# Kernel tuning notes

Measured on AMD Instinct MI355X. Metric: run time of the kernel, lower is better.

The kernel has to match this reference:

```python
import jax, jax.numpy as jnp
import numpy as np

B, NG, GS, D, L, NDL = 16, 50, 20, 256, 3, 2
N = NG * GS  # 1000


def setup_inputs() -> dict:
    key = jax.random.key(0)
    ks = jax.random.split(key, 8)
    amino_embd = jax.random.normal(ks[0], (B, NG, GS, D), dtype=jnp.float32)
    c = (jax.random.uniform(ks[1], (B, N, N)) < 0.02).astype(jnp.float32)
    prot_contacts = jnp.clip(c + jnp.transpose(c, (0, 2, 1)), 0.0, 1.0)
    # small init for bilinear W (original: random_uniform ~ +/-0.05) keeps exp() stable
    W_list = 0.01 * jax.random.normal(ks[2], (L, D, D), dtype=jnp.float32)
    dense_W = jax.random.normal(ks[3], (L, NDL, D, D), dtype=jnp.float32) / np.sqrt(D)
    dense_b = jnp.zeros((L, NDL, D), dtype=jnp.float32)
    final_W = jax.random.normal(ks[4], (D, D), dtype=jnp.float32) / np.sqrt(D)
    final_b = jnp.zeros((D,), dtype=jnp.float32)
    return {"amino_embd": amino_embd, "prot_contacts": prot_contacts,
            "W_list": W_list, "dense_W": dense_W, "dense_b": dense_b,
            "final_W": final_W, "final_b": final_b}


def reference(amino_embd, prot_contacts, W_list, dense_W, dense_b, final_W, final_b):
    dt = amino_embd.dtype
    eye = jnp.eye(N, dtype=dt)
    A = prot_contacts + eye  # contact map with self loops, [B,N,N]
    x = amino_embd.reshape(B, N, D)
    for l in range(L):
        x0 = x
        # bilinear non-local scores: [B,N,N]
        scores = jnp.einsum('bid,de,bje->bij', x0, W_list[l], x0)
        s = jnp.exp(scores) + jnp.asarray(1e-5, dt) * eye
        s = s * A                                   # mask by contacts + self loop
        s = s / jnp.sum(s, axis=-1, keepdims=True)  # row-normalize
        x = jnp.einsum('bij,bjd->bid', s, x0)       # aggregate
        for dl in range(NDL):
            x = jax.nn.relu(x @ dense_W[l, dl] + dense_b[l, dl])
        x = x + x0  # skip connection
    x = x @ final_W + final_b
    return x.reshape(B, NG, GS, D)
```

## Files before the change

### kernel.cpp

```cpp
#include <hip/hip_runtime.h>

#define BB 16
#define NN 1000
#define DD 256
#define LL 3
#define MAXNZ 256
#define MROWS (BB * NN)
#define SPLIT_SCALE 2048.0f
#define INV_SPLIT 4.8828125e-4f

typedef _Float16 f16x8 __attribute__((ext_vector_type(8)));
typedef _Float16 f16x2 __attribute__((ext_vector_type(2)));
typedef float f32x4 __attribute__((ext_vector_type(4)));

union H8 { f16x8 v; f16x2 p[4]; _Float16 h[8]; int4 i4; };

#if defined(__has_builtin)
#if __has_builtin(__builtin_amdgcn_fdot2)
#define HAS_FDOT2 1
#endif
#endif

__device__ __forceinline__ float dot2f(f16x2 a, f16x2 b, float c) {
#ifdef HAS_FDOT2
    return __builtin_amdgcn_fdot2(a, b, c, false);
#else
    return fmaf((float)a[0], (float)b[0], fmaf((float)a[1], (float)b[1], c));
#endif
}

__global__ __launch_bounds__(256) void convert_w(
    const float* __restrict__ W_list, const float* __restrict__ dense_W,
    const float* __restrict__ final_W,
    _Float16* __restrict__ wt_hi, _Float16* __restrict__ wt_lo)
{
    __shared__ float T[64][68];
    int blk = blockIdx.x;
    int mat = blk >> 4;
    int tile = blk & 15;
    int tk = (tile >> 2) * 64, tn = (tile & 3) * 64;
    const float* src = (mat < 3) ? (W_list + (size_t)mat * 65536)
                     : (mat < 9) ? (dense_W + (size_t)(mat - 3) * 65536)
                                 : final_W;
    int t = threadIdx.x;
    {
        int k = t >> 2, nc = (t & 3) * 16;
        const float* sp = src + (size_t)(tk + k) * 256 + tn + nc;
        *(float4*)&T[k][nc + 0]  = *(const float4*)(sp + 0);
        *(float4*)&T[k][nc + 4]  = *(const float4*)(sp + 4);
        *(float4*)&T[k][nc + 8]  = *(const float4*)(sp + 8);
        *(float4*)&T[k][nc + 12] = *(const float4*)(sp + 12);
    }
    __syncthreads();
    int n = t >> 2, kc = (t & 3) * 16;
    H8 hh0, hh1, ll0, ll1;
    #pragma unroll
    for (int i = 0; i < 16; ++i) {
        float x = T[kc + i][n];
        _Float16 hi = (_Float16)x;
        _Float16 lo = (_Float16)((x - (float)hi) * SPLIT_SCALE);
        if (i < 8) { hh0.h[i] = hi; ll0.h[i] = lo; }
        else       { hh1.h[i - 8] = hi; ll1.h[i - 8] = lo; }
    }
    size_t o = (size_t)mat * 65536 + (size_t)(tn + n) * 256 + tk + kc;
    *(int4*)(wt_hi + o)     = hh0.i4;
    *(int4*)(wt_hi + o + 8) = hh1.i4;
    *(int4*)(wt_lo + o)     = ll0.i4;
    *(int4*)(wt_lo + o + 8) = ll1.i4;
}

__global__ __launch_bounds__(256) void convert_x(
    const float* __restrict__ in, _Float16* __restrict__ hi,
    _Float16* __restrict__ lo)
{
    size_t gid = (size_t)blockIdx.x * 256 + threadIdx.x;
    const float* p = in + gid * 8;
    float4 a = *(const float4*)p;
    float4 b = *(const float4*)(p + 4);
    float xs[8] = {a.x, a.y, a.z, a.w, b.x, b.y, b.z, b.w};
    H8 hh, ll;
    #pragma unroll
    for (int i = 0; i < 8; ++i) {
        _Float16 h = (_Float16)xs[i];
        hh.h[i] = h;
        ll.h[i] = (_Float16)((xs[i] - (float)h) * SPLIT_SCALE);
    }
    *(int4*)(hi + gid * 8) = hh.i4;
    *(int4*)(lo + gid * 8) = ll.i4;
}

__global__ __launch_bounds__(256) void build_sparse(
    const float* __restrict__ contacts,
    int* __restrict__ idx, int* __restrict__ cnt, float* __restrict__ adiag)
{
    int wave = (int)((blockIdx.x * blockDim.x + threadIdx.x) >> 6);
    int lane = threadIdx.x & 63;
    if (wave >= MROWS) return;
    int b = wave / NN;
    int i = wave - b * NN;
    const float* row = contacts + (size_t)b * NN * NN + (size_t)i * NN;
    int* out = idx + (size_t)wave * MAXNZ;
    int count = 0;
    for (int j0 = 0; j0 < NN; j0 += 64) {
        int j = j0 + lane;
        float v = (j < NN) ? row[j] : 0.0f;
        bool p = (v != 0.0f) && (j != i);
        unsigned long long bal = __ballot(p);
        if (p) {
            int pre = __popcll(bal & ((1ull << lane) - 1ull));
            out[count + pre] = j;
        }
        count += __popcll(bal);
    }
    if (lane == 0) {
        cnt[wave] = count;
        adiag[wave] = row[i] + 1.0f;
    }
}

__global__ __launch_bounds__(256) void sparse_agg(
    const _Float16* __restrict__ yhi,
    const _Float16* __restrict__ xhi, const _Float16* __restrict__ xlo,
    const int* __restrict__ idx, const int* __restrict__ cnt,
    const float* __restrict__ adiag,
    _Float16* __restrict__ ohi, _Float16* __restrict__ olo)
{
    int bid = blockIdx.x;
    int xcd = bid & 7;
    int chunk = bid >> 3;
    int row = xcd * 2000 + chunk * 4 + (int)(threadIdx.x >> 6);
    row = __builtin_amdgcn_readfirstlane(row);
    int lane = threadIdx.x & 63;
    int g = lane >> 4, s = lane & 15;
    int b = row / NN;

    const _Float16* yp = yhi + (size_t)row * DD + s * 8;
    H8 yh0, yh1;
    yh0.i4 = *(const int4*)yp;
    yh1.i4 = *(const int4*)(yp + 128);

    const _Float16* xph = xhi + (size_t)row * DD + s * 8;
    const _Float16* xpl = xlo + (size_t)row * DD + s * 8;
    H8 xih0, xih1, xil0, xil1;
    xih0.i4 = *(const int4*)xph;       xih1.i4 = *(const int4*)(xph + 128);
    xil0.i4 = *(const int4*)xpl;       xil1.i4 = *(const int4*)(xpl + 128);
    float xi[16];
    #pragma unroll
    for (int u = 0; u < 8; ++u) {
        xi[u]     = fmaf((float)xil0.h[u], INV_SPLIT, (float)xih0.h[u]);
        xi[8 + u] = fmaf((float)xil1.h[u], INV_SPLIT, (float)xih1.h[u]);
    }
    const _Float16* xb = xhi + (size_t)b * NN * DD;

    float p = 0.0f;
    #pragma unroll
    for (int u = 0; u < 8; ++u) {
        p = fmaf((float)yh0.h[u], xi[u], p);
        p = fmaf((float)yh1.h[u], xi[8 + u], p);
    }
    p += __shfl_xor(p, 1); p += __shfl_xor(p, 2);
    p += __shfl_xor(p, 4); p += __shfl_xor(p, 8);
    float wd = (g == 0) ? (__expf(p) + 1e-5f) * adiag[row] : 0.0f;
    float denom = wd;
    float acc[16];
    #pragma unroll
    for (int u = 0; u < 16; ++u) acc[u] = wd * xi[u];

    const int c = cnt[row];
    const int* ip = idx + (size_t)row * MAXNZ;
    const int iters = (c + 3) >> 2;

    int j0 = (g < c) ? ip[g] : 0;
    int j1 = (4 + g < c) ? ip[4 + g] : 0;
    bool vok = g < c;
    H8 v0, v1;
    {
        const _Float16* xp = xb + (size_t)j0 * DD + s * 8;
        v0.i4 = *(const int4*)xp;
        v1.i4 = *(const int4*)(xp + 128);
    }

    for (int t = 0; t < iters; ++t) {
        int k2 = (t + 2) * 4 + g;
        int j2 = (k2 < c) ? ip[k2] : 0;
        H8 n0, n1;
        const _Float16* np = xb + (size_t)j1 * DD + s * 8;
        n0.i4 = *(const int4*)np;
        n1.i4 = *(const int4*)(np + 128);

        float q = 0.0f;
        #pragma unroll
        for (int i = 0; i < 4; ++i) q = dot2f(yh0.p[i], v0.p[i], q);
        #pragma unroll
        for (int i = 0; i < 4; ++i) q = dot2f(yh1.p[i], v1.p[i], q);
        q += __shfl_xor(q, 1); q += __shfl_xor(q, 2);
        q += __shfl_xor(q, 4); q += __shfl_xor(q, 8);
        float w = vok ? __expf(q) : 0.0f;
        denom += w;
        #pragma unroll
        for (int u = 0; u < 8; ++u) {
            acc[u]     = fmaf(w, (float)v0.h[u], acc[u]);
            acc[8 + u] = fmaf(w, (float)v1.h[u], acc[8 + u]);
        }

        v0 = n0; v1 = n1;
        j1 = j2;
        vok = (t + 1) * 4 + g < c;
    }

#define XG(x) x += __shfl_xor(x, 16); x += __shfl_xor(x, 32);
    XG(denom);
    #pragma unroll
    for (int u = 0; u < 16; ++u) { XG(acc[u]) }
#undef XG

    float inv = 1.0f / denom;
    int half = (g & 1) * 8;
    H8 st;
    #pragma unroll
    for (int i = 0; i < 8; ++i) {
        float x = acc[half + i] * inv;
        _Float16 h = (_Float16)x;
        st.h[i] = (g & 2) ? (_Float16)((x - (float)h) * SPLIT_SCALE) : h;
    }
    _Float16* dst = ((g & 2) ? olo : ohi) + (size_t)row * DD + (g & 1) * 128 + s * 8;
    *(int4*)dst = st.i4;
}

__global__ __launch_bounds__(256, 3) void gemm16(
    const _Float16* __restrict__ Ahi, const _Float16* __restrict__ Alo,
    const _Float16* __restrict__ Bhi, const _Float16* __restrict__ Blo,
    const float* __restrict__ bias,
    const _Float16* __restrict__ Shi, const _Float16* __restrict__ Slo,
    _Float16* __restrict__ Chi, _Float16* __restrict__ Clo,
    float* __restrict__ Cf32, int relu)
{
    __shared__ __align__(16) char smem[49152];
    char* Ah = smem;
    char* Al = smem + 8192;
    char* Bh = smem + 16384;
    char* Bl = smem + 32768;

    int tid = threadIdx.x;
    int mBase = blockIdx.y * 64;
    int nBase = blockIdx.x * 128;

    int sm = tid >> 2, kc = (tid & 3) * 16;
    int sb = tid >> 1, kcb = (tid & 1) * 32;
    const _Float16* gAh = Ahi + (size_t)(mBase + sm) * 256 + kc;
    const _Float16* gAl = Alo + (size_t)(mBase + sm) * 256 + kc;
    const _Float16* gBh = Bhi + (size_t)(nBase + sb) * 256 + kcb;
    const _Float16* gBl = Blo + (size_t)(nBase + sb) * 256 + kcb;
    int sbA = sm * 128 + kc * 2, swzA = (sm & 7) << 4;
    int sbB = sb * 128 + kcb * 2, swzB = (sb & 7) << 4;

    int l = tid & 63, wv = tid >> 6;
    int wm = (wv & 1) * 32, wn = (wv >> 1) * 64;
    int lr = l & 15, lkb = (l >> 4) * 16;

    f32x4 acc0[2][4] = {};
    f32x4 acc1[2][4] = {};

    for (int kb = 0; kb < 256; kb += 64) {
        int4 ah0 = *(const int4*)(gAh + kb);
        int4 ah1 = *(const int4*)(gAh + kb + 8);
        int4 al0 = *(const int4*)(gAl + kb);
        int4 al1 = *(const int4*)(gAl + kb + 8);
        int4 bh0 = *(const int4*)(gBh + kb);
        int4 bh1 = *(const int4*)(gBh + kb + 8);
        int4 bh2 = *(const int4*)(gBh + kb + 16);
        int4 bh3 = *(const int4*)(gBh + kb + 24);
        int4 bl0 = *(const int4*)(gBl + kb);
        int4 bl1 = *(const int4*)(gBl + kb + 8);
        int4 bl2 = *(const int4*)(gBl + kb + 16);
        int4 bl3 = *(const int4*)(gBl + kb + 24);

        __syncthreads();
        *(int4*)(Ah + ((sbA +  0) ^ swzA)) = ah0;
        *(int4*)(Ah + ((sbA + 16) ^ swzA)) = ah1;
        *(int4*)(Al + ((sbA +  0) ^ swzA)) = al0;
        *(int4*)(Al + ((sbA + 16) ^ swzA)) = al1;
        *(int4*)(Bh + ((sbB +  0) ^ swzB)) = bh0;
        *(int4*)(Bh + ((sbB + 16) ^ swzB)) = bh1;
        *(int4*)(Bh + ((sbB + 32) ^ swzB)) = bh2;
        *(int4*)(Bh + ((sbB + 48) ^ swzB)) = bh3;
        *(int4*)(Bl + ((sbB +  0) ^ swzB)) = bl0;
        *(int4*)(Bl + ((sbB + 16) ^ swzB)) = bl1;
        *(int4*)(Bl + ((sbB + 32) ^ swzB)) = bl2;
        *(int4*)(Bl + ((sbB + 48) ^ swzB)) = bl3;
        __syncthreads();

        #pragma unroll
        for (int kk = 0; kk < 2; ++kk) {
            int kby = kk * 64 + lkb;
            f16x8 fah[2], fal[2];
            #pragma unroll
            for (int mt = 0; mt < 2; ++mt) {
                int ml = wm + mt * 16 + lr;
                int off = (ml * 128 + kby) ^ ((ml & 7) << 4);
                fah[mt] = *(const f16x8*)(Ah + off);
                fal[mt] = *(const f16x8*)(Al + off);
            }
            f16x8 fbh[4], fbl[4];
            #pragma unroll
            for (int nt = 0; nt < 4; ++nt) {
                int nl = wn + nt * 16 + lr;
                int off = (nl * 128 + kby) ^ ((nl & 7) << 4);
                fbh[nt] = *(const f16x8*)(Bh + off);
                fbl[nt] = *(const f16x8*)(Bl + off);
            }
            #pragma unroll
            for (int mt = 0; mt < 2; ++mt)
                #pragma unroll
                for (int nt = 0; nt < 4; ++nt) {
                    acc0[mt][nt] = __builtin_amdgcn_mfma_f32_16x16x32_f16(
                        fah[mt], fbh[nt], acc0[mt][nt], 0, 0, 0);
                    acc1[mt][nt] = __builtin_amdgcn_mfma_f32_16x16x32_f16(
                        fah[mt], fbl[nt], acc1[mt][nt], 0, 0, 0);
                    acc1[mt][nt] = __builtin_amdgcn_mfma_f32_16x16x32_f16(
                        fal[mt], fbh[nt], acc1[mt][nt], 0, 0, 0);
                }
        }
    }

    #pragma unroll
    for (int mt = 0; mt < 2; ++mt) {
        #pragma unroll
        for (int nt = 0; nt < 4; ++nt) {
            int n = nBase + wn + nt * 16 + lr;
            float bv = bias ? bias[n] : 0.0f;
            #pragma unroll
            for (int q = 0; q < 4; ++q) {
                int m = mBase + wm + mt * 16 + (l >> 4) * 4 + q;
                size_t o = (size_t)m * 256 + n;
                float v = acc0[mt][nt][q] + acc1[mt][nt][q] * INV_SPLIT + bv;
                if (relu) v = fmaxf(v, 0.0f);
                if (Shi) v += (float)Shi[o] + (float)Slo[o] * INV_SPLIT;
                if (Cf32) {
                    Cf32[o] = v;
                } else {
                    _Float16 h = (_Float16)v;
                    Chi[o] = h;
                    Clo[o] = (_Float16)((v - (float)h) * SPLIT_SCALE);
                }
            }
        }
    }
}

extern "C" void kernel_launch(void* const* d_in, const int* in_sizes, int n_in,
                              void* d_out, int out_size, void* d_ws, size_t ws_size,
                              hipStream_t stream)
{
    const float* x_in     = (const float*)d_in[0];
    const float* contacts = (const float*)d_in[1];
    const float* W_list   = (const float*)d_in[2];
    const float* dense_W  = (const float*)d_in[3];
    const float* dense_b  = (const float*)d_in[4];
    const float* final_W  = (const float*)d_in[5];
    const float* final_b  = (const float*)d_in[6];
    float* out = (float*)d_out;

    char* ws = (char*)d_ws;
    const size_t PL = (size_t)MROWS * DD;
    _Float16* pl[8];
    for (int i = 0; i < 8; ++i) pl[i] = (_Float16*)ws + (size_t)i * PL;
    char* p8 = ws + 8 * PL * sizeof(_Float16);
    int*   idx   = (int*)p8;
    int*   cnt   = (int*)(p8 + (size_t)MROWS * MAXNZ * sizeof(int));
    float* adiag = (float*)((char*)cnt + (size_t)MROWS * sizeof(int));
    _Float16* wt_hi = (_Float16*)((char*)adiag + (size_t)MROWS * sizeof(float));
    _Float16* wt_lo = wt_hi + (size_t)10 * 65536;

    convert_w<<<160, 256, 0, stream>>>(W_list, dense_W, final_W, wt_hi, wt_lo);
    convert_x<<<MROWS * DD / (256 * 8), 256, 0, stream>>>(x_in, pl[0], pl[1]);
    build_sparse<<<MROWS / 4, 256, 0, stream>>>(contacts, idx, cnt, adiag);

    dim3 gg(2, MROWS / 64);
    int cur = 0;
    for (int l = 0; l < LL; ++l) {
        int oth = 1 - cur;
        _Float16 *x0h = pl[2 * cur], *x0l = pl[2 * cur + 1];
        _Float16 *yh  = pl[2 * oth], *yl  = pl[2 * oth + 1];
        _Float16 *xah = pl[4], *xal = pl[5];
        _Float16 *xbh = pl[6], *xbl = pl[7];
        gemm16<<<gg, 256, 0, stream>>>(x0h, x0l,
                                       wt_hi + (size_t)l * 65536,
                                       wt_lo + (size_t)l * 65536,
                                       nullptr, nullptr, nullptr,
                                       yh, yl, nullptr, 0);
        sparse_agg<<<MROWS / 4, 256, 0, stream>>>(yh, x0h, x0l, idx, cnt, adiag,
                                                  xah, xal);
        gemm16<<<gg, 256, 0, stream>>>(xah, xal,
                                       wt_hi + (size_t)(3 + l * 2) * 65536,
                                       wt_lo + (size_t)(3 + l * 2) * 65536,
                                       dense_b + (size_t)(l * 2 + 0) * 256,
                                       nullptr, nullptr,
                                       xbh, xbl, nullptr, 1);
        gemm16<<<gg, 256, 0, stream>>>(xbh, xbl,
                                       wt_hi + (size_t)(4 + l * 2) * 65536,
                                       wt_lo + (size_t)(4 + l * 2) * 65536,
                                       dense_b + (size_t)(l * 2 + 1) * 256,
                                       x0h, x0l,
                                       yh, yl, nullptr, 1);
        cur = oth;
    }
    gemm16<<<gg, 256, 0, stream>>>(pl[2 * cur], pl[2 * cur + 1],
                                   wt_hi + (size_t)9 * 65536,
                                   wt_lo + (size_t)9 * 65536,
                                   final_b, nullptr, nullptr,
                                   nullptr, nullptr, out, 0);
}
```

Measured before the change: 295.1 us.

## Split sparse aggregation rows across two waves and prefetch GEMM tiles

sparse_agg now assigns two waves per row, each handling alternate groups of neighbours, and combines their partial sums and denominators through shared memory before the write. This doubles the grid and halves each wave's serial neighbour loop to expose more memory parallelism. gemm16 also register-prefetches the next K tile's global loads while the current tile runs MFMA, and drops the launch-bounds occupancy hint from 3 to 2. The costs are an extra block barrier and LDS reduction in the aggregation kernel and higher register pressure in the GEMM.

```diff
diff --git a/kernel.cpp b/kernel.cpp
--- a/kernel.cpp
+++ b/kernel.cpp
@@ -125,10 +125,14 @@
     const float* __restrict__ adiag,
     _Float16* __restrict__ ohi, _Float16* __restrict__ olo)
 {
+    __shared__ float red[2][257];
     int bid = blockIdx.x;
     int xcd = bid & 7;
     int chunk = bid >> 3;
-    int row = xcd * 2000 + chunk * 4 + (int)(threadIdx.x >> 6);
+    int w = (int)(threadIdx.x >> 6);
+    int rib = w >> 1;
+    int h = w & 1;
+    int row = xcd * 2000 + chunk * 2 + rib;
     row = __builtin_amdgcn_readfirstlane(row);
     int lane = threadIdx.x & 63;
     int g = lane >> 4, s = lane & 15;
@@ -138,41 +142,50 @@
     H8 yh0, yh1;
     yh0.i4 = *(const int4*)yp;
     yh1.i4 = *(const int4*)(yp + 128);
-
-    const _Float16* xph = xhi + (size_t)row * DD + s * 8;
-    const _Float16* xpl = xlo + (size_t)row * DD + s * 8;
-    H8 xih0, xih1, xil0, xil1;
-    xih0.i4 = *(const int4*)xph;       xih1.i4 = *(const int4*)(xph + 128);
-    xil0.i4 = *(const int4*)xpl;       xil1.i4 = *(const int4*)(xpl + 128);
-    float xi[16];
-    #pragma unroll
-    for (int u = 0; u < 8; ++u) {
-        xi[u]     = fmaf((float)xil0.h[u], INV_SPLIT, (float)xih0.h[u]);
-        xi[8 + u] = fmaf((float)xil1.h[u], INV_SPLIT, (float)xih1.h[u]);
-    }
     const _Float16* xb = xhi + (size_t)b * NN * DD;
 
-    float p = 0.0f;
-    #pragma unroll
-    for (int u = 0; u < 8; ++u) {
-        p = fmaf((float)yh0.h[u], xi[u], p);
-        p = fmaf((float)yh1.h[u], xi[8 + u], p);
-    }
-    p += __shfl_xor(p, 1); p += __shfl_xor(p, 2);
-    p += __shfl_xor(p, 4); p += __shfl_xor(p, 8);
-    float wd = (g == 0) ? (__expf(p) + 1e-5f) * adiag[row] : 0.0f;
-    float denom = wd;
+    float denom = 0.0f;
     float acc[16];
     #pragma unroll
-    for (int u = 0; u < 16; ++u) acc[u] = wd * xi[u];
+    for (int u = 0; u < 16; ++u) acc[u] = 0.0f;
+
+    if (h == 0) {
+        const _Float16* xph = xhi + (size_t)row * DD + s * 8;
+        const _Float16* xpl = xlo + (size_t)row * DD + s * 8;
+        H8 xih0, xih1, xil0, xil1;
+        xih0.i4 = *(const int4*)xph;   xih1.i4 = *(const int4*)(xph + 128);
+        xil0.i4 = *(const int4*)xpl;   xil1.i4 = *(const int4*)(xpl + 128);
+        float xi[16];
+        #pragma unroll
+        for (int u = 0; u < 8; ++u) {
+            xi[u]     = fmaf((float)xil0.h[u], INV_SPLIT, (float)xih0.h[u]);
+            xi[8 + u] = fmaf((float)xil1.h[u], INV_SPLIT, (float)xih1.h[u]);
+        }
+        float p = 0.0f;
+        #pragma unroll
+        for (int u = 0; u < 8; ++u) {
+            p = fmaf((float)yh0.h[u], xi[u], p);
+            p = fmaf((float)yh1.h[u], xi[8 + u], p);
+        }
+        p += __shfl_xor(p, 1); p += __shfl_xor(p, 2);
+        p += __shfl_xor(p, 4); p += __shfl_xor(p, 8);
+        float wd = (g == 0) ? (__expf(p) + 1e-5f) * adiag[row] : 0.0f;
+        denom = wd;
+        #pragma unroll
+        for (int u = 0; u < 16; ++u)
+            acc[u] = wd * ((u < 8) ? xi[u] : xi[u]);
+        #pragma unroll
+        for (int u = 0; u < 16; ++u) acc[u] = wd * xi[u];
+    }
 
     const int c = cnt[row];
     const int* ip = idx + (size_t)row * MAXNZ;
-    const int iters = (c + 3) >> 2;
-
-    int j0 = (g < c) ? ip[g] : 0;
-    int j1 = (4 + g < c) ? ip[4 + g] : 0;
-    bool vok = g < c;
+    const int pbase = 2 * g + h;
+    const int iters = (c + 7) >> 3;
+
+    int j0 = (pbase < c) ? ip[pbase] : 0;
+    int j1 = (8 + pbase < c) ? ip[8 + pbase] : 0;
+    bool vok = pbase < c;
     H8 v0, v1;
     {
         const _Float16* xp = xb + (size_t)j0 * DD + s * 8;
@@ -181,7 +194,7 @@
     }
 
     for (int t = 0; t < iters; ++t) {
-        int k2 = (t + 2) * 4 + g;
+        int k2 = (t + 2) * 8 + pbase;
         int j2 = (k2 < c) ? ip[k2] : 0;
         H8 n0, n1;
         const _Float16* np = xb + (size_t)j1 * DD + s * 8;
@@ -195,17 +208,17 @@
         for (int i = 0; i < 4; ++i) q = dot2f(yh1.p[i], v1.p[i], q);
         q += __shfl_xor(q, 1); q += __shfl_xor(q, 2);
         q += __shfl_xor(q, 4); q += __shfl_xor(q, 8);
-        float w = vok ? __expf(q) : 0.0f;
-        denom += w;
+        float wq = vok ? __expf(q) : 0.0f;
+        denom += wq;
         #pragma unroll
         for (int u = 0; u < 8; ++u) {
-            acc[u]     = fmaf(w, (float)v0.h[u], acc[u]);
-            acc[8 + u] = fmaf(w, (float)v1.h[u], acc[8 + u]);
+            acc[u]     = fmaf(wq, (float)v0.h[u], acc[u]);
+            acc[8 + u] = fmaf(wq, (float)v1.h[u], acc[8 + u]);
         }
 
         v0 = n0; v1 = n1;
         j1 = j2;
-        vok = (t + 1) * 4 + g < c;
+        vok = (t + 1) * 8 + pbase < c;
     }
 
 #define XG(x) x += __shfl_xor(x, 16); x += __shfl_xor(x, 32);
@@ -214,20 +227,38 @@
     for (int u = 0; u < 16; ++u) { XG(acc[u]) }
 #undef XG
 
-    float inv = 1.0f / denom;
-    int half = (g & 1) * 8;
-    H8 st;
-    #pragma unroll
-    for (int i = 0; i < 8; ++i) {
-        float x = acc[half + i] * inv;
-        _Float16 h = (_Float16)x;
-        st.h[i] = (g & 2) ? (_Float16)((x - (float)h) * SPLIT_SCALE) : h;
-    }
-    _Float16* dst = ((g & 2) ? olo : ohi) + (size_t)row * DD + (g & 1) * 128 + s * 8;
-    *(int4*)dst = st.i4;
-}
-
-__global__ __launch_bounds__(256, 3) void gemm16(
+    if (h == 1 && g == 0) {
+        #pragma unroll
+        for (int u = 0; u < 8; ++u) {
+            red[rib][s * 8 + u]       = acc[u];
+            red[rib][128 + s * 8 + u] = acc[8 + u];
+        }
+        if (s == 0) red[rib][256] = denom;
+    }
+    __syncthreads();
+    if (h == 0) {
+        #pragma unroll
+        for (int u = 0; u < 8; ++u) {
+            acc[u]     += red[rib][s * 8 + u];
+            acc[8 + u] += red[rib][128 + s * 8 + u];
+        }
+        denom += red[rib][256];
+
+        float inv = 1.0f / denom;
+        int half = (g & 1) * 8;
+        H8 st;
+        #pragma unroll
+        for (int i = 0; i < 8; ++i) {
+            float x = acc[half + i] * inv;
+            _Float16 hh = (_Float16)x;
+            st.h[i] = (g & 2) ? (_Float16)((x - (float)hh) * SPLIT_SCALE) : hh;
+        }
+        _Float16* dst = ((g & 2) ? olo : ohi) + (size_t)row * DD + (g & 1) * 128 + s * 8;
+        *(int4*)dst = st.i4;
+    }
+}
+
+__global__ __launch_bounds__(256, 2) void gemm16(
     const _Float16* __restrict__ Ahi, const _Float16* __restrict__ Alo,
     const _Float16* __restrict__ Bhi, const _Float16* __restrict__ Blo,
     const float* __restrict__ bias,
@@ -261,34 +292,36 @@
     f32x4 acc0[2][4] = {};
     f32x4 acc1[2][4] = {};
 
+    int4 rA0, rA1, rA2, rA3;
+    int4 rB0, rB1, rB2, rB3, rB4, rB5, rB6, rB7;
+#define LOADG(kb) \
+    rA0 = *(const int4*)(gAh + (kb));      rA1 = *(const int4*)(gAh + (kb) + 8);  \
+    rA2 = *(const int4*)(gAl + (kb));      rA3 = *(const int4*)(gAl + (kb) + 8);  \
+    rB0 = *(const int4*)(gBh + (kb));      rB1 = *(const int4*)(gBh + (kb) + 8);  \
+    rB2 = *(const int4*)(gBh + (kb) + 16); rB3 = *(const int4*)(gBh + (kb) + 24); \
+    rB4 = *(const int4*)(gBl + (kb));      rB5 = *(const int4*)(gBl + (kb) + 8);  \
+    rB6 = *(const int4*)(gBl + (kb) + 16); rB7 = *(const int4*)(gBl + (kb) + 24);
+
+    LOADG(0)
+
+    #pragma unroll
     for (int kb = 0; kb < 256; kb += 64) {
-        int4 ah0 = *(const int4*)(gAh + kb);
-        int4 ah1 = *(const int4*)(gAh + kb + 8);
-        int4 al0 = *(const int4*)(gAl + kb);
-        int4 al1 = *(const int4*)(gAl + kb + 8);
-        int4 bh0 = *(const int4*)(gBh + kb);
-        int4 bh1 = *(const int4*)(gBh + kb + 8);
-        int4 bh2 = *(const int4*)(gBh + kb + 16);
-        int4 bh3 = *(const int4*)(gBh + kb + 24);
-        int4 bl0 = *(const int4*)(gBl + kb);
-        int4 bl1 = *(const int4*)(gBl + kb + 8);
-        int4 bl2 = *(const int4*)(gBl + kb + 16);
-        int4 bl3 = *(const int4*)(gBl + kb + 24);
-
         __syncthreads();
-        *(int4*)(Ah + ((sbA +  0) ^ swzA)) = ah0;
-        *(int4*)(Ah + ((sbA + 16) ^ swzA)) = ah1;
-        *(int4*)(Al + ((sbA +  0) ^ swzA)) = al0;
-        *(int4*)(Al + ((sbA + 16) ^ swzA)) = al1;
-        *(int4*)(Bh + ((sbB +  0) ^ swzB)) = bh0;
-        *(int4*)(Bh + ((sbB + 16) ^ swzB)) = bh1;
-        *(int4*)(Bh + ((sbB + 32) ^ swzB)) = bh2;
-        *(int4*)(Bh + ((sbB + 48) ^ swzB)) = bh3;
-        *(int4*)(Bl + ((sbB +  0) ^ swzB)) = bl0;
-        *(int4*)(Bl + ((sbB + 16) ^ swzB)) = bl1;
-        *(int4*)(Bl + ((sbB + 32) ^ swzB)) = bl2;
-        *(int4*)(Bl + ((sbB + 48) ^ swzB)) = bl3;
+        *(int4*)(Ah + ((sbA +  0) ^ swzA)) = rA0;
+        *(int4*)(Ah + ((sbA + 16) ^ swzA)) = rA1;
+        *(int4*)(Al + ((sbA +  0) ^ swzA)) = rA2;
+        *(int4*)(Al + ((sbA + 16) ^ swzA)) = rA3;
+        *(int4*)(Bh + ((sbB +  0) ^ swzB)) = rB0;
+        *(int4*)(Bh + ((sbB + 16) ^ swzB)) = rB1;
+        *(int4*)(Bh + ((sbB + 32) ^ swzB)) = rB2;
+        *(int4*)(Bh + ((sbB + 48) ^ swzB)) = rB3;
+        *(int4*)(Bl + ((sbB +  0) ^ swzB)) = rB4;
+        *(int4*)(Bl + ((sbB + 16) ^ swzB)) = rB5;
+        *(int4*)(Bl + ((sbB + 32) ^ swzB)) = rB6;
+        *(int4*)(Bl + ((sbB + 48) ^ swzB)) = rB7;
         __syncthreads();
+
+        if (kb < 192) { LOADG(kb + 64) }
 
         #pragma unroll
         for (int kk = 0; kk < 2; ++kk) {
@@ -322,6 +355,7 @@
                 }
         }
     }
+#undef LOADG
 
     #pragma unroll
     for (int mt = 0; mt < 2; ++mt) {
@@ -339,9 +373,9 @@
                 if (Cf32) {
                     Cf32[o] = v;
                 } else {
-                    _Float16 h = (_Float16)v;
-                    Chi[o] = h;
-                    Clo[o] = (_Float16)((v - (float)h) * SPLIT_SCALE);
+                    _Float16 hh = (_Float16)v;
+                    Chi[o] = hh;
+                    Clo[o] = (_Float16)((v - (float)hh) * SPLIT_SCALE);
                 }
             }
         }
@@ -389,7 +423,7 @@
                                        wt_lo + (size_t)l * 65536,
                                        nullptr, nullptr, nullptr,
                                        yh, yl, nullptr, 0);
-        sparse_agg<<<MROWS / 4, 256, 0, stream>>>(yh, x0h, x0l, idx, cnt, adiag,
+        sparse_agg<<<MROWS / 2, 256, 0, stream>>>(yh, x0h, x0l, idx, cnt, adiag,
                                                   xah, xal);
         gemm16<<<gg, 256, 0, stream>>>(xah, xal,
                                        wt_hi + (size_t)(3 + l * 2) * 65536,
```

Result: slower. 306.0 us (+3.7%).

## Restructure GEMM: full-K A tile in LDS, direct B register loads, staged epilogue

Applied to the files above, without the earlier changes.

The gemm16 kernel now loads the whole 64x256 A tile (hi and lo) into shared memory once. B fragments are read straight from global memory into registers, with the next k-step prefetched, which removes the per-k-block LDS staging and its barriers. The epilogue writes accumulators to an LDS transpose buffer so that bias, relu, residual and output stores can use vectorized 16-byte accesses instead of scalar ones. In exchange, shared memory grows to 64KB and occupancy drops to 2 blocks, and B is reloaded from global (or cache) by every wave that needs it.

```diff
diff --git a/kernel.cpp b/kernel.cpp
--- a/kernel.cpp
+++ b/kernel.cpp
@@ -227,7 +227,7 @@
     *(int4*)dst = st.i4;
 }
 
-__global__ __launch_bounds__(256, 3) void gemm16(
+__global__ __launch_bounds__(256, 2) void gemm16(
     const _Float16* __restrict__ Ahi, const _Float16* __restrict__ Alo,
     const _Float16* __restrict__ Bhi, const _Float16* __restrict__ Blo,
     const float* __restrict__ bias,
@@ -235,114 +235,154 @@
     _Float16* __restrict__ Chi, _Float16* __restrict__ Clo,
     float* __restrict__ Cf32, int relu)
 {
-    __shared__ __align__(16) char smem[49152];
+    __shared__ __align__(16) char smem[65536];
     char* Ah = smem;
-    char* Al = smem + 8192;
-    char* Bh = smem + 16384;
-    char* Bl = smem + 32768;
+    char* Al = smem + 32768;
 
     int tid = threadIdx.x;
     int mBase = blockIdx.y * 64;
     int nBase = blockIdx.x * 128;
 
-    int sm = tid >> 2, kc = (tid & 3) * 16;
-    int sb = tid >> 1, kcb = (tid & 1) * 32;
-    const _Float16* gAh = Ahi + (size_t)(mBase + sm) * 256 + kc;
-    const _Float16* gAl = Alo + (size_t)(mBase + sm) * 256 + kc;
-    const _Float16* gBh = Bhi + (size_t)(nBase + sb) * 256 + kcb;
-    const _Float16* gBl = Blo + (size_t)(nBase + sb) * 256 + kcb;
-    int sbA = sm * 128 + kc * 2, swzA = (sm & 7) << 4;
-    int sbB = sb * 128 + kcb * 2, swzB = (sb & 7) << 4;
+    {
+        int r = tid & 63;
+        int kc = (tid >> 6) * 64;
+        const _Float16* pAh = Ahi + (size_t)(mBase + r) * 256 + kc;
+        const _Float16* pAl = Alo + (size_t)(mBase + r) * 256 + kc;
+        int base = r * 512 + kc * 2;
+        int swz = (r & 7) << 4;
+        #pragma unroll
+        for (int i = 0; i < 8; ++i) {
+            *(int4*)(Ah + ((base + i * 16) ^ swz)) = *(const int4*)(pAh + i * 8);
+            *(int4*)(Al + ((base + i * 16) ^ swz)) = *(const int4*)(pAl + i * 8);
+        }
+    }
+    __syncthreads();
 
     int l = tid & 63, wv = tid >> 6;
     int wm = (wv & 1) * 32, wn = (wv >> 1) * 64;
-    int lr = l & 15, lkb = (l >> 4) * 16;
+    int lr = l & 15, lk = l >> 4;
+
+    const _Float16* bh[4];
+    const _Float16* bl[4];
+    #pragma unroll
+    for (int nt = 0; nt < 4; ++nt) {
+        size_t ro = (size_t)(nBase + wn + nt * 16 + lr) * 256 + lk * 8;
+        bh[nt] = Bhi + ro;
+        bl[nt] = Blo + ro;
+    }
 
     f32x4 acc0[2][4] = {};
     f32x4 acc1[2][4] = {};
 
-    for (int kb = 0; kb < 256; kb += 64) {
-        int4 ah0 = *(const int4*)(gAh + kb);
-        int4 ah1 = *(const int4*)(gAh + kb + 8);
-        int4 al0 = *(const int4*)(gAl + kb);
-        int4 al1 = *(const int4*)(gAl + kb + 8);
-        int4 bh0 = *(const int4*)(gBh + kb);
-        int4 bh1 = *(const int4*)(gBh + kb + 8);
-        int4 bh2 = *(const int4*)(gBh + kb + 16);
-        int4 bh3 = *(const int4*)(gBh + kb + 24);
-        int4 bl0 = *(const int4*)(gBl + kb);
-        int4 bl1 = *(const int4*)(gBl + kb + 8);
-        int4 bl2 = *(const int4*)(gBl + kb + 16);
-        int4 bl3 = *(const int4*)(gBl + kb + 24);
-
-        __syncthreads();
-        *(int4*)(Ah + ((sbA +  0) ^ swzA)) = ah0;
-        *(int4*)(Ah + ((sbA + 16) ^ swzA)) = ah1;
-        *(int4*)(Al + ((sbA +  0) ^ swzA)) = al0;
-        *(int4*)(Al + ((sbA + 16) ^ swzA)) = al1;
-        *(int4*)(Bh + ((sbB +  0) ^ swzB)) = bh0;
-        *(int4*)(Bh + ((sbB + 16) ^ swzB)) = bh1;
-        *(int4*)(Bh + ((sbB + 32) ^ swzB)) = bh2;
-        *(int4*)(Bh + ((sbB + 48) ^ swzB)) = bh3;
-        *(int4*)(Bl + ((sbB +  0) ^ swzB)) = bl0;
-        *(int4*)(Bl + ((sbB + 16) ^ swzB)) = bl1;
-        *(int4*)(Bl + ((sbB + 32) ^ swzB)) = bl2;
-        *(int4*)(Bl + ((sbB + 48) ^ swzB)) = bl3;
-        __syncthreads();
-
-        #pragma unroll
-        for (int kk = 0; kk < 2; ++kk) {
-            int kby = kk * 64 + lkb;
-            f16x8 fah[2], fal[2];
-            #pragma unroll
-            for (int mt = 0; mt < 2; ++mt) {
-                int ml = wm + mt * 16 + lr;
-                int off = (ml * 128 + kby) ^ ((ml & 7) << 4);
-                fah[mt] = *(const f16x8*)(Ah + off);
-                fal[mt] = *(const f16x8*)(Al + off);
-            }
-            f16x8 fbh[4], fbl[4];
+    H8 nb[8];
+    #pragma unroll
+    for (int nt = 0; nt < 4; ++nt) {
+        nb[nt].i4     = *(const int4*)(bh[nt]);
+        nb[4 + nt].i4 = *(const int4*)(bl[nt]);
+    }
+
+    #pragma unroll
+    for (int s = 0; s < 8; ++s) {
+        H8 cb[8];
+        #pragma unroll
+        for (int i = 0; i < 8; ++i) cb[i] = nb[i];
+        if (s < 7) {
             #pragma unroll
             for (int nt = 0; nt < 4; ++nt) {
-                int nl = wn + nt * 16 + lr;
-                int off = (nl * 128 + kby) ^ ((nl & 7) << 4);
-                fbh[nt] = *(const f16x8*)(Bh + off);
-                fbl[nt] = *(const f16x8*)(Bl + off);
-            }
-            #pragma unroll
-            for (int mt = 0; mt < 2; ++mt)
+                nb[nt].i4     = *(const int4*)(bh[nt] + (s + 1) * 32);
+                nb[4 + nt].i4 = *(const int4*)(bl[nt] + (s + 1) * 32);
+            }
+        }
+        f16x8 fah[2], fal[2];
+        #pragma unroll
+        for (int mt = 0; mt < 2; ++mt) {
+            int ml = wm + mt * 16 + lr;
+            int off = (ml * 512 + s * 64 + lk * 16) ^ ((ml & 7) << 4);
+            fah[mt] = *(const f16x8*)(Ah + off);
+            fal[mt] = *(const f16x8*)(Al + off);
+        }
+        #pragma unroll
+        for (int mt = 0; mt < 2; ++mt)
+            #pragma unroll
+            for (int nt = 0; nt < 4; ++nt) {
+                acc0[mt][nt] = __builtin_amdgcn_mfma_f32_16x16x32_f16(
+                    fah[mt], cb[nt].v, acc0[mt][nt], 0, 0, 0);
+                acc1[mt][nt] = __builtin_amdgcn_mfma_f32_16x16x32_f16(
+                    fah[mt], cb[4 + nt].v, acc1[mt][nt], 0, 0, 0);
+                acc1[mt][nt] = __builtin_amdgcn_mfma_f32_16x16x32_f16(
+                    fal[mt], cb[nt].v, acc1[mt][nt], 0, 0, 0);
+            }
+    }
+
+    __syncthreads();
+    float* T = (float*)smem;
+    #pragma unroll
+    for (int mt = 0; mt < 2; ++mt)
+        #pragma unroll
+        for (int nt = 0; nt < 4; ++nt)
+            #pragma unroll
+            for (int q = 0; q < 4; ++q) {
+                int m = wm + mt * 16 + lk * 4 + q;
+                int n = wn + nt * 16 + lr;
+                T[m * 132 + n] = acc0[mt][nt][q] + acc1[mt][nt][q] * INV_SPLIT;
+            }
+    __syncthreads();
+
+    {
+        int r = tid >> 2;
+        int c0 = (tid & 3) * 32;
+        int m = mBase + r;
+        int n0 = nBase + c0;
+        float v[32];
+        #pragma unroll
+        for (int i = 0; i < 8; ++i) {
+            float4 f = *(const float4*)&T[r * 132 + c0 + i * 4];
+            v[i * 4 + 0] = f.x; v[i * 4 + 1] = f.y;
+            v[i * 4 + 2] = f.z; v[i * 4 + 3] = f.w;
+        }
+        if (bias) {
+            #pragma unroll
+            for (int i = 0; i < 8; ++i) {
+                float4 bv = *(const float4*)(bias + n0 + i * 4);
+                v[i * 4 + 0] += bv.x; v[i * 4 + 1] += bv.y;
+                v[i * 4 + 2] += bv.z; v[i * 4 + 3] += bv.w;
+            }
+        }
+        if (relu) {
+            #pragma unroll
+            for (int i = 0; i < 32; ++i) v[i] = fmaxf(v[i], 0.0f);
+        }
+        size_t o = (size_t)m * 256 + n0;
+        if (Shi) {
+            #pragma unroll
+            for (int j = 0; j < 4; ++j) {
+                H8 sh, sl;
+                sh.i4 = *(const int4*)(Shi + o + j * 8);
+                sl.i4 = *(const int4*)(Slo + o + j * 8);
                 #pragma unroll
-                for (int nt = 0; nt < 4; ++nt) {
-                    acc0[mt][nt] = __builtin_amdgcn_mfma_f32_16x16x32_f16(
-                        fah[mt], fbh[nt], acc0[mt][nt], 0, 0, 0);
-                    acc1[mt][nt] = __builtin_amdgcn_mfma_f32_16x16x32_f16(
-                        fah[mt], fbl[nt], acc1[mt][nt], 0, 0, 0);
-                    acc1[mt][nt] = __builtin_amdgcn_mfma_f32_16x16x32_f16(
-                        fal[mt], fbh[nt], acc1[mt][nt], 0, 0, 0);
+                for (int u = 0; u < 8; ++u)
+                    v[j * 8 + u] += fmaf((float)sl.h[u], INV_SPLIT, (float)sh.h[u]);
+            }
+        }
+        if (Cf32) {
+            #pragma unroll
+            for (int i = 0; i < 8; ++i) {
+                float4 f = make_float4(v[i * 4], v[i * 4 + 1], v[i * 4 + 2], v[i * 4 + 3]);
+                *(float4*)(Cf32 + o + i * 4) = f;
+            }
+        } else {
+            #pragma unroll
+            for (int j = 0; j < 4; ++j) {
+                H8 hh, ll;
+                #pragma unroll
+                for (int u = 0; u < 8; ++u) {
+                    float x = v[j * 8 + u];
+                    _Float16 h = (_Float16)x;
+                    hh.h[u] = h;
+                    ll.h[u] = (_Float16)((x - (float)h) * SPLIT_SCALE);
                 }
-        }
-    }
-
-    #pragma unroll
-    for (int mt = 0; mt < 2; ++mt) {
-        #pragma unroll
-        for (int nt = 0; nt < 4; ++nt) {
-            int n = nBase + wn + nt * 16 + lr;
-            float bv = bias ? bias[n] : 0.0f;
-            #pragma unroll
-            for (int q = 0; q < 4; ++q) {
-                int m = mBase + wm + mt * 16 + (l >> 4) * 4 + q;
-                size_t o = (size_t)m * 256 + n;
-                float v = acc0[mt][nt][q] + acc1[mt][nt][q] * INV_SPLIT + bv;
-                if (relu) v = fmaxf(v, 0.0f);
-                if (Shi) v += (float)Shi[o] + (float)Slo[o] * INV_SPLIT;
-                if (Cf32) {
-                    Cf32[o] = v;
-                } else {
-                    _Float16 h = (_Float16)v;
-                    Chi[o] = h;
-                    Clo[o] = (_Float16)((v - (float)h) * SPLIT_SCALE);
-                }
+                *(int4*)(Chi + o + j * 8) = hh.i4;
+                *(int4*)(Clo + o + j * 8) = ll.i4;
             }
         }
     }
```

Result: slower. 411.0 us (+39.3%).
